# Performance work log

Hardware: AMD Instinct MI355X
Metric: run time of the kernel (lower is better)

## Reference

```python
import jax, jax.numpy as jnp
import numpy as np

N = 65536   # batch
G = 7       # grid
C = 2       # classes (cats vs dogs)
A = 3       # anchors


def _bce(p, t):
    return -(t * jnp.log(p) + (1.0 - t) * jnp.log(1.0 - p))


def _iou(a, b):
    # a, b: [..., 4] boxes in (cx, cy, w, h) format
    ax1, ay1 = a[..., 0] - a[..., 2] / 2, a[..., 1] - a[..., 3] / 2
    ax2, ay2 = a[..., 0] + a[..., 2] / 2, a[..., 1] + a[..., 3] / 2
    bx1, by1 = b[..., 0] - b[..., 2] / 2, b[..., 1] - b[..., 3] / 2
    bx2, by2 = b[..., 0] + b[..., 2] / 2, b[..., 1] + b[..., 3] / 2
    iw = jnp.clip(jnp.minimum(ax2, bx2) - jnp.maximum(ax1, bx1), 0.0)
    ih = jnp.clip(jnp.minimum(ay2, by2) - jnp.maximum(ay1, by1), 0.0)
    inter = iw * ih
    union = (ax2 - ax1) * (ay2 - ay1) + (bx2 - bx1) * (by2 - by1) - inter
    return inter / (union + 1e-9)


def setup_inputs():
    key = jax.random.key(0)
    k1, k2, k3, k4 = jax.random.split(key, 4)
    # probabilities / box params must lie strictly in (0,1) for BCE and log()
    bbox_ = jax.random.uniform(k1, (N, 15, G, G), dtype=jnp.float32, minval=0.01, maxval=0.99)
    bbox = jax.random.uniform(k2, (N, 5, G, G), dtype=jnp.float32, minval=0.01, maxval=0.99)
    cls_ = jax.random.normal(k3, (N, C), dtype=jnp.float32)
    cls = jax.random.randint(k4, (N,), 1, 3).astype(jnp.int64)  # labels in {1,2}
    return {"bbox_": bbox_, "cls_": cls_, "bbox": bbox, "cls": cls}


def reference(bbox_, cls_, bbox, cls):
    n = bbox.shape[0]
    bidx = jnp.arange(n)

    # classification: CrossEntropyLoss (mean) with labels cls-1
    logp = jax.nn.log_softmax(cls_, axis=-1)
    ce = -jnp.mean(jnp.take_along_axis(logp, (cls - 1)[:, None], axis=1))

    # argmax cell of GT objectness map per sample
    probs = bbox[:, 0]                       # [N,7,7]
    m = jnp.argmax(probs.reshape(n, -1), axis=1)
    i, j = m // G, m % G                     # [N], [N]

    cell_gt = bbox[bidx, :, i, j]            # [N,5]
    cell_pr = bbox_[bidx, :, i, j].reshape(n, A, 5)  # [N,3,5]

    jf = j.astype(bbox.dtype)
    if_ = i.astype(bbox.dtype)

    # target box in global coords
    tgt = jnp.stack([(cell_gt[:, 1] + jf) / G, (cell_gt[:, 2] + if_) / G,
                     cell_gt[:, 3], cell_gt[:, 4]], axis=-1)          # [N,4]
    # anchor boxes in global coords
    anc = jnp.stack([(cell_pr[:, :, 1] + jf[:, None]) / G,
                     (cell_pr[:, :, 2] + if_[:, None]) / G,
                     cell_pr[:, :, 3], cell_pr[:, :, 4]], axis=-1)    # [N,3,4]

    best = jnp.argmax(_iou(anc, tgt[:, None, :]), axis=1)             # [N]

    # target objectness maps: best anchor channel gets GT prob map
    target_prob = jnp.zeros((n, A, G, G), dtype=bbox.dtype)
    target_prob = target_prob.at[bidx, best].set(probs)

    # coordinate BCE (sum) + size L1-of-logs (sum) at the matched cell/anchor
    best_box = cell_pr[bidx, best]           # [N,5]
    coord = jnp.sum(_bce(best_box[:, 1:3], cell_gt[:, 1:3]))
    size = jnp.sum(jnp.abs(jnp.log(best_box[:, 3:5]) - jnp.log(cell_gt[:, 3:5])))

    # per-anchor objectness BCE (mean over N*49 each)
    prob_loss = (jnp.mean(_bce(bbox_[:, 0], target_prob[:, 0]))
                 + jnp.mean(_bce(bbox_[:, 5], target_prob[:, 1]))
                 + jnp.mean(_bce(bbox_[:, 10], target_prob[:, 2])))

    return ce + coord + size + prob_loss
```

## Files before the change

kernel.cpp:

```cpp
#include <hip/hip_runtime.h>
#include <math.h>


static constexpr int GG_ = 49;
static constexpr int PRD = 15 * GG_;
static constexpr int GTD = 5  * GG_;

__global__ void zero_kernel(float* out) { if (threadIdx.x == 0) out[0] = 0.0f; }

__global__ __launch_bounds__(256) void loss_kernel(
    const float* __restrict__ pr_all,
    const float* __restrict__ cls_logits,
    const float* __restrict__ gt_all,
    const int*   __restrict__ cls_lbl,
    float* __restrict__ out, int N)
{
    const int lane   = threadIdx.x & 63;
    const int wslot  = threadIdx.x >> 6;
    const int wid    = blockIdx.x * (blockDim.x >> 6) + wslot;
    const int nwaves = gridDim.x * (blockDim.x >> 6);
    const float invG   = 1.0f / 7.0f;
    const float invN   = 1.0f / (float)N;
    const float invN49 = 1.0f / ((float)N * 49.0f);

    __shared__ float lds_pr[4][768];
    __shared__ float lds_gt[4][256];
    float* __restrict__ Lpr = lds_pr[wslot];
    float* __restrict__ Lgt = lds_gt[wslot];

    float acc = 0.0f;

    for (int n = wid; n < N; n += nwaves) {
        const float* pr = pr_all + (size_t)n * PRD;
        const float* gt = gt_all + (size_t)n * GTD;

        float p[12];
        #pragma unroll
        for (int k = 0; k < 12; k++) {
            int d = lane + 64 * k;
            if (d > PRD - 1) d = PRD - 1;
            p[k] = pr[d];
        }
        float g[4];
        #pragma unroll
        for (int k = 0; k < 4; k++) {
            int d = lane + 64 * k;
            if (d > GTD - 1) d = GTD - 1;
            g[k] = gt[d];
        }
        const float x0 = cls_logits[2 * n];
        const float x1 = cls_logits[2 * n + 1];
        const int   c  = cls_lbl[n] - 1;

        #pragma unroll
        for (int k = 0; k < 12; k++) Lpr[lane + 64 * k] = p[k];
        #pragma unroll
        for (int k = 0; k < 4;  k++) Lgt[lane + 64 * k] = g[k];
        asm volatile("s_waitcnt lgkmcnt(0)" ::: "memory");

        const float t = (lane < GG_) ? g[0] : -1.0f;
        float v = t; int idx = lane;
        #pragma unroll
        for (int off = 32; off; off >>= 1) {
            float v2 = __shfl_xor(v, off);
            int   i2 = __shfl_xor(idx, off);
            if (v2 > v || (v2 == v && i2 < idx)) { v = v2; idx = i2; }
        }
        const int m  = idx;
        const int mi = m / 7, mj = m - mi * 7;
        const float jf = (float)mj, if_ = (float)mi;

        const float g1 = Lgt[ 49 + m];
        const float g2 = Lgt[ 98 + m];
        const float g3 = Lgt[147 + m];
        const float g4 = Lgt[196 + m];

        const float tx  = (g1 + jf) * invG;
        const float ty  = (g2 + if_) * invG;
        const float tx1 = tx - g3 * 0.5f, tx2 = tx + g3 * 0.5f;
        const float ty1 = ty - g4 * 0.5f, ty2 = ty + g4 * 0.5f;
        const float tarea = (tx2 - tx1) * (ty2 - ty1);

        int best = 0; float bestIoU = -1.0f;
        float px = 0.f, py = 0.f, pw = 0.f, ph = 0.f;
        #pragma unroll
        for (int a = 0; a < 3; a++) {
            float c1 = Lpr[(5 * a + 1) * GG_ + m];
            float c2 = Lpr[(5 * a + 2) * GG_ + m];
            float c3 = Lpr[(5 * a + 3) * GG_ + m];
            float c4 = Lpr[(5 * a + 4) * GG_ + m];
            float ax  = (c1 + jf) * invG;
            float ay  = (c2 + if_) * invG;
            float ax1 = ax - c3 * 0.5f, ax2 = ax + c3 * 0.5f;
            float ay1 = ay - c4 * 0.5f, ay2 = ay + c4 * 0.5f;
            float iw = fminf(ax2, tx2) - fmaxf(ax1, tx1); iw = fmaxf(iw, 0.0f);
            float ih = fminf(ay2, ty2) - fmaxf(ay1, ty1); ih = fmaxf(ih, 0.0f);
            float inter = iw * ih;
            float uni   = (ax2 - ax1) * (ay2 - ay1) + tarea - inter;
            float iou   = inter / (uni + 1e-9f);
            if (iou > bestIoU) { bestIoU = iou; best = a; px = c1; py = c2; pw = c3; ph = c4; }
        }

        float s = 0.0f;
        if (lane < 49) s -= __logf(1.0f - p[0]);
        if (lane >= 53) s -= __logf(1.0f - p[3]);
        if (lane < 38) s -= __logf(1.0f - p[4]);
        if (lane >= 42) s -= __logf(1.0f - p[7]);
        if (lane < 27) s -= __logf(1.0f - p[8]);

        if (lane < GG_) {
            float pb = Lpr[245 * best + lane];
            s -= t * (__logf(pb) - __logf(1.0f - pb));
        }
        acc += s * invN49;

        if (lane == 0) {
            float coord = -(g1 * __logf(px) + (1.0f - g1) * __logf(1.0f - px))
                          -(g2 * __logf(py) + (1.0f - g2) * __logf(1.0f - py));
            float size  = fabsf(__logf(pw) - __logf(g3))
                        + fabsf(__logf(ph) - __logf(g4));
            float mx  = fmaxf(x0, x1);
            float lse = mx + __logf(__expf(x0 - mx) + __expf(x1 - mx));
            float lp  = ((c == 0) ? x0 : x1) - lse;
            acc += coord + size - lp * invN;
        }
    }

    #pragma unroll
    for (int off = 32; off; off >>= 1) acc += __shfl_xor(acc, off);
    __shared__ float wsum[4];
    if (lane == 0) wsum[wslot] = acc;
    __syncthreads();
    if (threadIdx.x == 0) {
        atomicAdd(out, wsum[0] + wsum[1] + wsum[2] + wsum[3]);
    }
}

extern "C" void kernel_launch(void* const* d_in, const int* in_sizes, int n_in,
                              void* d_out, int out_size, void* d_ws, size_t ws_size,
                              hipStream_t stream) {
    const float* bbox_p = (const float*)d_in[0];
    const float* cls_p  = (const float*)d_in[1];
    const float* bbox_g = (const float*)d_in[2];
    const int*   cls_l  = (const int*)d_in[3];
    float* out = (float*)d_out;
    const int N = in_sizes[3];

    hipLaunchKernelGGL(zero_kernel, dim3(1), dim3(64), 0, stream, out);
    hipLaunchKernelGGL(loss_kernel, dim3(2048), dim3(256), 0, stream,
                       bbox_p, cls_p, bbox_g, cls_l, out, N);
}
```

Before: 314.5 us.

## Double-buffer sample groups into LDS via async global_load_lds prefetch

Replaces per-wave register loads followed by LDS stores with direct global-to-LDS 16-byte async loads covering four contiguous samples per block. The next group is staged into a second buffer while the current one is processed, so memory latency overlaps compute. It also simplifies the argmax to a max-reduce plus ballot, cuts redundant logs by reusing log(1-p), and spreads the per-sample scalar logs across lanes. In exchange each group now needs a block-wide barrier, and samples are assigned to blocks as contiguous chunks.

Result: no change. 317.4 us (+0.9%).

```diff
diff --git a/kernel.cpp b/kernel.cpp
--- a/kernel.cpp
+++ b/kernel.cpp
@@ -2,11 +2,39 @@
 #include <math.h>
 
 
-static constexpr int GG_ = 49;
-static constexpr int PRD = 15 * GG_;
-static constexpr int GTD = 5  * GG_;
+static constexpr int GG  = 49;
+static constexpr int PRD = 15 * GG;
+static constexpr int GTD = 5  * GG;
+static constexpr int SPG = 4;
+static constexpr int PRC = SPG * PRD;
+static constexpr int GTC = SPG * GTD;
+static constexpr int PRB = PRC * 4;
+static constexpr int GTB = GTC * 4;
 
 __global__ void zero_kernel(float* out) { if (threadIdx.x == 0) out[0] = 0.0f; }
+
+__device__ __forceinline__ void gload16(const float* g, float* l) {
+    __builtin_amdgcn_global_load_lds(
+        (const __attribute__((address_space(1))) void*)g,
+        (__attribute__((address_space(3))) void*)l, 16, 0, 0);
+}
+
+__device__ __forceinline__ void stage_group(const float* __restrict__ prs,
+                                            const float* __restrict__ gts,
+                                            float* buf, int wslot, int lane) {
+    #pragma unroll
+    for (int u0 = 0; u0 < 3; ++u0) {
+        const int u   = wslot + 4 * u0;
+        const int rem = PRB - (u << 10);
+        if ((lane << 4) < rem)
+            gload16(prs + (u << 8) + (lane << 2), buf + (u << 8));
+    }
+    {   const int u   = wslot;
+        const int rem = GTB - (u << 10);
+        if ((lane << 4) < rem)
+            gload16(gts + (u << 8) + (lane << 2), buf + PRC + (u << 8));
+    }
+}
 
 __global__ __launch_bounds__(256) void loss_kernel(
     const float* __restrict__ pr_all,
@@ -15,115 +43,125 @@
     const int*   __restrict__ cls_lbl,
     float* __restrict__ out, int N)
 {
-    const int lane   = threadIdx.x & 63;
-    const int wslot  = threadIdx.x >> 6;
-    const int wid    = blockIdx.x * (blockDim.x >> 6) + wslot;
-    const int nwaves = gridDim.x * (blockDim.x >> 6);
+    const int lane  = threadIdx.x & 63;
+    const int wslot = threadIdx.x >> 6;
     const float invG   = 1.0f / 7.0f;
     const float invN   = 1.0f / (float)N;
     const float invN49 = 1.0f / ((float)N * 49.0f);
 
-    __shared__ float lds_pr[4][768];
-    __shared__ float lds_gt[4][256];
-    float* __restrict__ Lpr = lds_pr[wslot];
-    float* __restrict__ Lgt = lds_gt[wslot];
+    __shared__ float L[2][PRC + GTC];
+
+    const int ngroups = N >> 2;
+    const int per = (ngroups + gridDim.x - 1) / gridDim.x;
+    const int gA  = blockIdx.x * per;
+    const int gB  = min(gA + per, ngroups);
 
     float acc = 0.0f;
+    int cur = 0;
 
-    for (int n = wid; n < N; n += nwaves) {
-        const float* pr = pr_all + (size_t)n * PRD;
-        const float* gt = gt_all + (size_t)n * GTD;
+    if (gA < gB)
+        stage_group(pr_all + (size_t)gA * PRC, gt_all + (size_t)gA * GTC,
+                    L[0], wslot, lane);
+    __syncthreads();
 
-        float p[12];
-        #pragma unroll
-        for (int k = 0; k < 12; k++) {
-            int d = lane + 64 * k;
-            if (d > PRD - 1) d = PRD - 1;
-            p[k] = pr[d];
-        }
-        float g[4];
-        #pragma unroll
-        for (int k = 0; k < 4; k++) {
-            int d = lane + 64 * k;
-            if (d > GTD - 1) d = GTD - 1;
-            g[k] = gt[d];
-        }
+    for (int g = gA; g < gB; ++g) {
+        const int n = (g << 2) + wslot;
+
         const float x0 = cls_logits[2 * n];
         const float x1 = cls_logits[2 * n + 1];
-        const int   c  = cls_lbl[n] - 1;
+        const int   cl = cls_lbl[n];
 
+        if (g + 1 < gB)
+            stage_group(pr_all + (size_t)(g + 1) * PRC,
+                        gt_all + (size_t)(g + 1) * GTC,
+                        L[cur ^ 1], wslot, lane);
+
+        const float* Lp = L[cur];
+        const float* Lg = L[cur] + PRC;
+        const int pb_ = wslot * PRD;
+        const int gb_ = wslot * GTD;
+
+        const float t = (lane < GG) ? Lg[gb_ + lane] : -1.0f;
+        float v = t;
         #pragma unroll
-        for (int k = 0; k < 12; k++) Lpr[lane + 64 * k] = p[k];
-        #pragma unroll
-        for (int k = 0; k < 4;  k++) Lgt[lane + 64 * k] = g[k];
-        asm volatile("s_waitcnt lgkmcnt(0)" ::: "memory");
-
-        const float t = (lane < GG_) ? g[0] : -1.0f;
-        float v = t; int idx = lane;
-        #pragma unroll
-        for (int off = 32; off; off >>= 1) {
-            float v2 = __shfl_xor(v, off);
-            int   i2 = __shfl_xor(idx, off);
-            if (v2 > v || (v2 == v && i2 < idx)) { v = v2; idx = i2; }
-        }
-        const int m  = idx;
+        for (int off = 32; off; off >>= 1) v = fmaxf(v, __shfl_xor(v, off));
+        const unsigned long long eq = __ballot(t == v);
+        const int m  = __ffsll(eq) - 1;
         const int mi = m / 7, mj = m - mi * 7;
         const float jf = (float)mj, if_ = (float)mi;
 
-        const float g1 = Lgt[ 49 + m];
-        const float g2 = Lgt[ 98 + m];
-        const float g3 = Lgt[147 + m];
-        const float g4 = Lgt[196 + m];
+        const float g1v = Lg[gb_ +  49 + m];
+        const float g2v = Lg[gb_ +  98 + m];
+        const float g3v = Lg[gb_ + 147 + m];
+        const float g4v = Lg[gb_ + 196 + m];
 
-        const float tx  = (g1 + jf) * invG;
-        const float ty  = (g2 + if_) * invG;
-        const float tx1 = tx - g3 * 0.5f, tx2 = tx + g3 * 0.5f;
-        const float ty1 = ty - g4 * 0.5f, ty2 = ty + g4 * 0.5f;
+        const float tx  = (g1v + jf) * invG;
+        const float ty  = (g2v + if_) * invG;
+        const float tx1 = tx - g3v * 0.5f, tx2 = tx + g3v * 0.5f;
+        const float ty1 = ty - g4v * 0.5f, ty2 = ty + g4v * 0.5f;
         const float tarea = (tx2 - tx1) * (ty2 - ty1);
 
         int best = 0; float bestIoU = -1.0f;
         float px = 0.f, py = 0.f, pw = 0.f, ph = 0.f;
         #pragma unroll
         for (int a = 0; a < 3; a++) {
-            float c1 = Lpr[(5 * a + 1) * GG_ + m];
-            float c2 = Lpr[(5 * a + 2) * GG_ + m];
-            float c3 = Lpr[(5 * a + 3) * GG_ + m];
-            float c4 = Lpr[(5 * a + 4) * GG_ + m];
-            float ax  = (c1 + jf) * invG;
-            float ay  = (c2 + if_) * invG;
-            float ax1 = ax - c3 * 0.5f, ax2 = ax + c3 * 0.5f;
-            float ay1 = ay - c4 * 0.5f, ay2 = ay + c4 * 0.5f;
+            const float c1 = Lp[pb_ + (5 * a + 1) * GG + m];
+            const float c2 = Lp[pb_ + (5 * a + 2) * GG + m];
+            const float c3 = Lp[pb_ + (5 * a + 3) * GG + m];
+            const float c4 = Lp[pb_ + (5 * a + 4) * GG + m];
+            const float ax  = (c1 + jf) * invG;
+            const float ay  = (c2 + if_) * invG;
+            const float ax1 = ax - c3 * 0.5f, ax2 = ax + c3 * 0.5f;
+            const float ay1 = ay - c4 * 0.5f, ay2 = ay + c4 * 0.5f;
             float iw = fminf(ax2, tx2) - fmaxf(ax1, tx1); iw = fmaxf(iw, 0.0f);
             float ih = fminf(ay2, ty2) - fmaxf(ay1, ty1); ih = fmaxf(ih, 0.0f);
-            float inter = iw * ih;
-            float uni   = (ax2 - ax1) * (ay2 - ay1) + tarea - inter;
-            float iou   = inter / (uni + 1e-9f);
+            const float inter = iw * ih;
+            const float uni   = (ax2 - ax1) * (ay2 - ay1) + tarea - inter;
+            const float iou   = inter / (uni + 1e-9f);
             if (iou > bestIoU) { bestIoU = iou; best = a; px = c1; py = c2; pw = c3; ph = c4; }
         }
 
         float s = 0.0f;
-        if (lane < 49) s -= __logf(1.0f - p[0]);
-        if (lane >= 53) s -= __logf(1.0f - p[3]);
-        if (lane < 38) s -= __logf(1.0f - p[4]);
-        if (lane >= 42) s -= __logf(1.0f - p[7]);
-        if (lane < 27) s -= __logf(1.0f - p[8]);
-
-        if (lane < GG_) {
-            float pb = Lpr[245 * best + lane];
-            s -= t * (__logf(pb) - __logf(1.0f - pb));
+        if (lane < GG) {
+            const float p0 = Lp[pb_ +           lane];
+            const float p1 = Lp[pb_ + 5 * GG  + lane];
+            const float p2 = Lp[pb_ + 10 * GG + lane];
+            const float l0 = __logf(1.0f - p0);
+            const float l1 = __logf(1.0f - p1);
+            const float l2 = __logf(1.0f - p2);
+            s = -(l0 + l1 + l2);
+            const float pbv  = (best == 0) ? p0 : (best == 1) ? p1 : p2;
+            const float l1pb = (best == 0) ? l0 : (best == 1) ? l1 : l2;
+            s -= t * (__logf(pbv) - l1pb);
         }
         acc += s * invN49;
 
-        if (lane == 0) {
-            float coord = -(g1 * __logf(px) + (1.0f - g1) * __logf(1.0f - px))
-                          -(g2 * __logf(py) + (1.0f - g2) * __logf(1.0f - py));
-            float size  = fabsf(__logf(pw) - __logf(g3))
-                        + fabsf(__logf(ph) - __logf(g4));
-            float mx  = fmaxf(x0, x1);
-            float lse = mx + __logf(__expf(x0 - mx) + __expf(x1 - mx));
-            float lp  = ((c == 0) ? x0 : x1) - lse;
-            acc += coord + size - lp * invN;
+        const float s0  = (lane < 4) ? ((lane < 2) ? px : py)
+                                     : ((lane < 6) ? pw : ph);
+        const float s1  = (lane < 4) ? (1.0f - s0)
+                                     : ((lane < 6) ? g3v : g4v);
+        const float la  = (lane & 1) ? s1 : s0;
+        const float Lv  = __logf(la);
+        const float Lx  = __shfl_xor(Lv, 1);
+        float contrib = 0.0f;
+        if (lane < 4) {
+            const float w = (lane < 2) ? ((lane & 1) ? 1.0f - g1v : g1v)
+                                       : ((lane & 1) ? 1.0f - g2v : g2v);
+            contrib = -w * Lv;
+        } else if (lane == 4 || lane == 6) {
+            contrib = fabsf(Lv - Lx);
         }
+        acc += contrib;
+
+        if (lane == 5) {
+            const float mx  = fmaxf(x0, x1);
+            const float lse = mx + __logf(1.0f + __expf(-fabsf(x0 - x1)));
+            const float lp  = ((cl == 1) ? x0 : x1) - lse;
+            acc -= lp * invN;
+        }
+
+        __syncthreads();
+        cur ^= 1;
     }
 
     #pragma unroll
```
